# Kernel tuning notes

Hardware: AMD Instinct MI355X
Metric: run time of the kernel (lower is better)

## Reference

```python
import jax, jax.numpy as jnp
import numpy as np

EPS = 1e-12  # tf.nn.l2_normalize epsilon used inside keras CosineSimilarity


def _cos(a, b):
    # keras CosineSimilarity returns -cos; callers negate explicitly.
    an = a / jnp.sqrt(jnp.maximum(jnp.sum(a * a, axis=-1, keepdims=True), EPS))
    bn = b / jnp.sqrt(jnp.maximum(jnp.sum(b * b, axis=-1, keepdims=True), EPS))
    return jnp.sum(an * bn, axis=-1)


def setup_inputs() -> dict:
    key = jax.random.key(0)
    B, S, D, H, N = 1024, 200, 128, 128, 64
    ks = jax.random.split(key, 8)
    X_series = jax.random.normal(ks[0], (B, S, D), jnp.float32)
    pos_series = jax.random.normal(ks[1], (S, D), jnp.float32)
    X_item = jax.random.normal(ks[2], (B, D), jnp.float32)
    origin = jax.random.normal(ks[3], (B, N, D), jnp.float32)  # X_negative
    # contiguous-prefix validity mask (module assumes valid positions form a prefix)
    lengths = jax.random.randint(ks[4], (B,), 1, S + 1)
    valid_mask = jnp.arange(S)[None, :] < lengths[:, None]
    # learned params (GlorotUniform-scale init)
    Wp = jax.random.normal(ks[5], (D, H), jnp.float32) * 0.08
    We = jax.random.normal(ks[6], (D, H), jnp.float32) * 0.08
    z = jax.random.normal(ks[7], (H,), jnp.float32) * 0.1
    return {"X_series": X_series, "pos_series": pos_series, "X_item": X_item,
            "valid_mask": valid_mask, "origin": origin, "Wp": Wp, "We": We, "z": z}


def reference(X_series, pos_series, X_item, valid_mask, origin, Wp, We, z):
    B, S, D = X_series.shape
    # additive tanh attention: z . tanh(X_series @ We + pos_series @ Wp)
    hidden = jnp.tanh(jnp.einsum('bsd,dh->bsh', X_series, We) + (pos_series @ Wp)[None])
    scores = jnp.einsum('bsh,h->bs', hidden, z)
    scores = jnp.where(valid_mask, scores, -jnp.inf)
    attn = jax.nn.softmax(scores, axis=-1)                      # [B,S]
    attentioned = attn[:, :, None] * X_series                    # [B,S,D]
    attention_output = jnp.sum(attentioned, axis=1)              # [B,D]
    inner = jnp.sum(attention_output * X_item, axis=-1, keepdims=True)
    concated = jnp.concatenate([attention_output, inner], axis=1)  # [B,D+1]

    # ---- auxiliary loss ----
    last_idx = jnp.sum(valid_mask.astype(jnp.int32), axis=1) - 1
    last_vec = attentioned[jnp.arange(B), last_idx]              # gather_nd
    new_mask = (jnp.arange(S)[None, :] < last_idx[:, None]).astype(X_series.dtype)
    out_vec = jnp.sum(attentioned * new_mask[:, :, None], axis=1)  # [B,D]
    # keras CosineSimilarity = -cos_sim; then mapped to (x+1)/2 and used as logits
    pos_logits = (-_cos(last_vec, out_vec) + 1.0) / 2.0          # [B]
    neg_logits = (-_cos(origin, out_vec[:, None, :]) + 1.0) / 2.0  # [B,N]
    pos_loss = jax.nn.softplus(-pos_logits)  # sigmoid_xent labels=1
    neg_loss = jax.nn.softplus(neg_logits)   # sigmoid_xent labels=0
    # NB: TF reduces pos_loss over its only axis -> scalar, broadcast-added to [B]
    auxiliary_loss = jnp.sum(pos_loss) + jnp.sum(neg_loss, axis=-1)  # [B]
    return concated, auxiliary_loss
```

## Files before the change

kernel.cpp:

```cpp
#include <hip/hip_runtime.h>
#include <hip/hip_bf16.h>
#include <math.h>

#define B_ 1024
#define S_ 200
#define D_ 128
#define H_ 128
#define N_ 64
#define SP_ 208

typedef __attribute__((ext_vector_type(8))) short short8;
typedef __attribute__((ext_vector_type(8))) __bf16 bf16x8;
typedef __attribute__((ext_vector_type(4))) float floatx4;

static __device__ __forceinline__ float bf2f(unsigned short u) {
    union { unsigned int i; float f; } v; v.i = ((unsigned int)u) << 16; return v.f;
}
static __device__ __forceinline__ unsigned short f2bf(float f) {
    union { float f; unsigned int u; } v; v.f = f;
    unsigned int u = v.u;
    return (unsigned short)((u + 0x7FFFu + ((u >> 16) & 1u)) >> 16);
}
static __device__ __forceinline__ float ld1(const void* p, int isbf, size_t i) {
    return isbf ? bf2f(((const unsigned short*)p)[i]) : ((const float*)p)[i];
}
static __device__ __forceinline__ float fast_tanh(float x) {
    float t = __expf(2.0f * x);
    return 1.0f - 2.0f * __builtin_amdgcn_rcpf(t + 1.0f);
}

__global__ __launch_bounds__(64) void detect_kernel(
    const void* a0, const void* a1, const void* a2, const void* a3,
    const void* a4, const void* a5, const void* a6, const void* a7,
    int* flags)
{
    int bid = blockIdx.x, t = threadIdx.x;
    if (bid == 3) {
        const unsigned char* mb = (const unsigned char*)a3;
        int f = 0;
        for (int i = t; i < 4096; i += 64)
            if ((i & 3) && mb[i]) f = 1;
        for (int off = 32; off; off >>= 1) f |= __shfl_xor(f, off, 64);
        if (t == 0) flags[3] = f;
        return;
    }
    const void* ptrs[8] = {a0, a1, a2, a3, a4, a5, a6, a7};
    const int counts[8] = {B_*S_*D_, S_*D_, B_*D_, 0, B_*N_*D_, D_*H_, D_*H_, H_};
    const unsigned int* w = (const unsigned int*)ptrs[bid];
    int words = counts[bid] / 2; if (words > 1024) words = 1024;
    int pass = 0, tot = 0;
    for (int i = t; i < words; i += 64) {
        unsigned int e = (w[i] >> 7) & 0xFF;
        tot++;
        if (e == 0 || (e >= 96 && e <= 140)) pass++;
    }
    for (int off = 32; off; off >>= 1) {
        pass += __shfl_xor(pass, off, 64);
        tot  += __shfl_xor(tot,  off, 64);
    }
    if (t == 0) flags[bid] = (pass * 4 >= tot * 3) ? 1 : 0;
}

__global__ __launch_bounds__(128) void prep_kernel(
    const void* __restrict__ We, const void* __restrict__ pos,
    const void* __restrict__ Wp, const int* __restrict__ flags,
    unsigned short* __restrict__ WeTf, float* __restrict__ pbT)
{
    int blk = blockIdx.x, t = threadIdx.x;
    __shared__ unsigned short T[128][136];
    __shared__ float prow[D_];
    if (blk == 0) {
        int fWe = flags[6];
        for (int c = t; c < 2048; c += 128) {
            int d = c >> 4, h8 = (c & 15) * 8;
            short8 v;
            if (fWe) {
                v = *(const short8*)((const unsigned short*)We + d * H_ + h8);
            } else {
                const float* p = (const float*)We + d * H_ + h8;
                float4 a = ((const float4*)p)[0], b = ((const float4*)p)[1];
                v[0] = (short)f2bf(a.x); v[1] = (short)f2bf(a.y);
                v[2] = (short)f2bf(a.z); v[3] = (short)f2bf(a.w);
                v[4] = (short)f2bf(b.x); v[5] = (short)f2bf(b.y);
                v[6] = (short)f2bf(b.z); v[7] = (short)f2bf(b.w);
            }
            *(short8*)(&T[d][h8]) = v;
        }
        __syncthreads();
        for (int i = t; i < 2048; i += 128) {
            int frag = i >> 6, ln = i & 63;
            int nt = frag >> 2, kks = frag & 3;
            int h = nt * 16 + (ln & 15);
            int dbase = kks * 32 + (ln >> 4) * 8;
            short8 v;
#pragma unroll
            for (int j = 0; j < 8; ++j) v[j] = (short)T[dbase + j][h];
            *(short8*)(WeTf + (size_t)i * 8) = v;
        }
        for (int i = t; i < H_ * (SP_ - S_); i += 128) {
            int h = i >> 3, s2 = S_ + (i & 7);
            pbT[(size_t)h * SP_ + s2] = 0.f;
        }
    } else {
        int s = blk - 1, h = t;
        prow[h] = ld1(pos, flags[1], (size_t)s * D_ + h);
        __syncthreads();
        float acc = 0.f;
        if (flags[5]) {
            const unsigned short* W = (const unsigned short*)Wp;
            for (int d = 0; d < D_; ++d) acc = fmaf(prow[d], bf2f(W[d * H_ + h]), acc);
        } else {
            const float* W = (const float*)Wp;
            for (int d = 0; d < D_; ++d) acc = fmaf(prow[d], W[d * H_ + h], acc);
        }
        pbT[(size_t)h * SP_ + s] = acc;
    }
}

__global__ __launch_bounds__(512, 4) void fused_kernel(
    const void* __restrict__ Xs, const void* __restrict__ Xitem,
    const void* __restrict__ maskv, const void* __restrict__ origin,
    const unsigned short* __restrict__ WeTf, const float* __restrict__ pbT,
    const void* __restrict__ zv, const int* __restrict__ flags,
    float* __restrict__ pos_loss, float* __restrict__ neg_sum,
    float* __restrict__ out)
{
    int b = blockIdx.x, t = threadIdx.x;
    int wv = t >> 6, lane = t & 63;
    int quad = lane >> 4, mrow = lane & 15;
    int fXs = flags[0], fXi = flags[2], fMk = flags[3], fOr = flags[4], fz = flags[7];

    __shared__ __align__(16) unsigned short Xsh[SP_ * D_];
    __shared__ float smemU[2048];
    __shared__ float attn[256];
    __shared__ float att_out[D_], lastv[D_], outv[D_];
    __shared__ float red[24];
    __shared__ int redi[8];
    __shared__ float sc1s, sc2s, vvs;

    int nn = t >> 3, part = t & 7;
    float o_f[16];
    if (fOr) {
        const unsigned short* p = (const unsigned short*)origin + ((size_t)b * N_ + nn) * D_ + part * 16;
#pragma unroll
        for (int j = 0; j < 2; ++j) {
            uint4 u = *(const uint4*)(p + j * 8);
            o_f[j*8+0] = bf2f((unsigned short)(u.x & 0xffff));
            o_f[j*8+1] = bf2f((unsigned short)(u.x >> 16));
            o_f[j*8+2] = bf2f((unsigned short)(u.y & 0xffff));
            o_f[j*8+3] = bf2f((unsigned short)(u.y >> 16));
            o_f[j*8+4] = bf2f((unsigned short)(u.z & 0xffff));
            o_f[j*8+5] = bf2f((unsigned short)(u.z >> 16));
            o_f[j*8+6] = bf2f((unsigned short)(u.w & 0xffff));
            o_f[j*8+7] = bf2f((unsigned short)(u.w >> 16));
        }
    } else {
        const float* p = (const float*)origin + ((size_t)b * N_ + nn) * D_ + part * 16;
#pragma unroll
        for (int j = 0; j < 4; ++j) {
            float4 v = *(const float4*)(p + j * 4);
            o_f[j*4+0] = v.x; o_f[j*4+1] = v.y; o_f[j*4+2] = v.z; o_f[j*4+3] = v.w;
        }
    }

    for (int i = t; i < SP_ * 16; i += 512) {
        int s = i >> 4, c8 = (i & 15) * 8;
        short8 v;
        if (s >= S_) {
#pragma unroll
            for (int j = 0; j < 8; ++j) v[j] = 0;
        } else if (fXs) {
            v = *(const short8*)((const unsigned short*)Xs + ((size_t)b * S_ + s) * D_ + c8);
        } else {
            const float* p = (const float*)Xs + ((size_t)b * S_ + s) * D_ + c8;
            float4 a = ((const float4*)p)[0], c = ((const float4*)p)[1];
            v[0] = (short)f2bf(a.x); v[1] = (short)f2bf(a.y);
            v[2] = (short)f2bf(a.z); v[3] = (short)f2bf(a.w);
            v[4] = (short)f2bf(c.x); v[5] = (short)f2bf(c.y);
            v[6] = (short)f2bf(c.z); v[7] = (short)f2bf(c.w);
        }
        *(short8*)(Xsh + s * D_ + (c8 ^ ((s & 7) << 3))) = v;
    }

    int nt = wv;
    bf16x8 bfr[4];
#pragma unroll
    for (int kks = 0; kks < 4; ++kks)
        bfr[kks] = __builtin_bit_cast(bf16x8,
            *(const short8*)(WeTf + (size_t)((((nt << 2) + kks) << 6) + lane) * 8));
    float zl = ld1(zv, fz, nt * 16 + mrow);
    const float* pbcol = pbT + (size_t)(nt * 16 + mrow) * SP_;

    __syncthreads();

    float* sp = smemU;
    for (int mt = 0; mt < 13; ++mt) {
        floatx4 acc = {0.f, 0.f, 0.f, 0.f};
        int r = mt * 16 + mrow;
        int rbase = r * D_, rx = (r & 7) << 3;
#pragma unroll
        for (int kks = 0; kks < 4; ++kks) {
            bf16x8 af = __builtin_bit_cast(bf16x8,
                *(const short8*)(Xsh + rbase + ((kks * 32 + quad * 8) ^ rx)));
            acc = __builtin_amdgcn_mfma_f32_16x16x32_bf16(af, bfr[kks], acc, 0, 0, 0);
        }
        float4 pbq = *(const float4*)(pbcol + mt * 16 + quad * 4);
#pragma unroll
        for (int reg = 0; reg < 4; ++reg) {
            float val = fast_tanh(acc[reg] + (&pbq.x)[reg]) * zl;
            val += __shfl_xor(val, 1, 64);
            val += __shfl_xor(val, 2, 64);
            val += __shfl_xor(val, 4, 64);
            val += __shfl_xor(val, 8, 64);
            int s = mt * 16 + quad * 4 + reg;
            if (mrow == 0 && s < S_) sp[nt * SP_ + s] = val;
        }
    }
    __syncthreads();

    float myscore = -INFINITY;
    if (t < S_) {
        float ss = 0.f;
#pragma unroll
        for (int w8 = 0; w8 < 8; ++w8) ss += sp[w8 * SP_ + t];
        myscore = ss;
    }

    int nz = 0;
    if (t < S_)
        nz = fMk ? (((const unsigned char*)maskv)[(size_t)b * S_ + t] != 0)
                 : (((const int*)maskv)[(size_t)b * S_ + t] != 0);
    unsigned long long bal = __ballot(nz);
    if (lane == 0) redi[wv] = __popcll(bal);
    __syncthreads();
    int length = redi[0] + redi[1] + redi[2] + redi[3]
               + redi[4] + redi[5] + redi[6] + redi[7];
    int last = length - 1;

    float sc = (t < length) ? myscore : -INFINITY;
    float m = sc;
    for (int off = 32; off; off >>= 1) m = fmaxf(m, __shfl_xor(m, off, 64));
    if (lane == 0) red[wv] = m;
    __syncthreads();
    if (t == 0) {
        float mm = red[0];
#pragma unroll
        for (int i = 1; i < 8; ++i) mm = fmaxf(mm, red[i]);
        sc1s = mm;
    }
    __syncthreads();
    float e = (t < length) ? expf(sc - sc1s) : 0.f;
    float rr = e;
    for (int off = 32; off; off >>= 1) rr += __shfl_xor(rr, off, 64);
    __syncthreads();
    if (lane == 0) red[wv] = rr;
    __syncthreads();
    if (t == 0) {
        float ssum = 0.f;
#pragma unroll
        for (int i = 0; i < 8; ++i) ssum += red[i];
        sc2s = ssum;
    }
    __syncthreads();
    if (t < 256) attn[t] = e / sc2s;
    __syncthreads();

    float* partial = smemU;
    {
        int spi = t >> 5, d4 = (t & 31) * 4;
        float a0 = 0.f, a1 = 0.f, a2 = 0.f, a3 = 0.f;
        if (fXs) {
            for (int s = spi; s < S_; s += 16) {
                float ww = attn[s];
                uint2 u = *(const uint2*)(Xsh + s * D_ + (d4 ^ ((s & 7) << 3)));
                a0 = fmaf(ww, bf2f((unsigned short)(u.x & 0xffff)), a0);
                a1 = fmaf(ww, bf2f((unsigned short)(u.x >> 16)), a1);
                a2 = fmaf(ww, bf2f((unsigned short)(u.y & 0xffff)), a2);
                a3 = fmaf(ww, bf2f((unsigned short)(u.y >> 16)), a3);
            }
        } else {
            for (int s = spi; s < S_; s += 16) {
                float ww = attn[s];
                float4 u = *(const float4*)((const float*)Xs + ((size_t)b * S_ + s) * D_ + d4);
                a0 = fmaf(ww, u.x, a0); a1 = fmaf(ww, u.y, a1);
                a2 = fmaf(ww, u.z, a2); a3 = fmaf(ww, u.w, a3);
            }
        }
        partial[spi * D_ + d4 + 0] = a0;
        partial[spi * D_ + d4 + 1] = a1;
        partial[spi * D_ + d4 + 2] = a2;
        partial[spi * D_ + d4 + 3] = a3;
    }
    __syncthreads();
    if (t < D_) {
        float v = 0.f;
#pragma unroll
        for (int p = 0; p < 16; ++p) v += partial[p * D_ + t];
        att_out[t] = v;
        float xl = fXs ? bf2f(Xsh[last * D_ + (t ^ ((last & 7) << 3))])
                       : ((const float*)Xs)[((size_t)b * S_ + last) * D_ + t];
        float lv = attn[last] * xl;
        lastv[t] = lv;
        outv[t] = v - lv;
    }
    __syncthreads();

    {
        float pi = (t < D_) ? att_out[t] * ld1(Xitem, fXi, (size_t)b * D_ + t) : 0.f;
        for (int off = 32; off; off >>= 1) pi += __shfl_xor(pi, off, 64);
        if (lane == 0) red[wv] = pi;
        __syncthreads();
        if (t < D_) out[(size_t)b * (D_ + 1) + t] = att_out[t];
        if (t == 0) {
            float s8 = 0.f;
#pragma unroll
            for (int i = 0; i < 8; ++i) s8 += red[i];
            out[(size_t)b * (D_ + 1) + D_] = s8;
        }
        __syncthreads();
    }

    {
        float l_ = (t < D_) ? lastv[t] : 0.f;
        float o_ = (t < D_) ? outv[t] : 0.f;
        float r0 = l_ * l_, r1 = l_ * o_, r2 = o_ * o_;
        for (int off = 32; off; off >>= 1) {
            r0 += __shfl_xor(r0, off, 64);
            r1 += __shfl_xor(r1, off, 64);
            r2 += __shfl_xor(r2, off, 64);
        }
        if (lane == 0) { red[wv] = r0; red[8 + wv] = r1; red[16 + wv] = r2; }
        __syncthreads();
        if (t == 0) {
            float ll = 0.f, lo = 0.f, oo = 0.f;
#pragma unroll
            for (int i = 0; i < 8; ++i) { ll += red[i]; lo += red[8 + i]; oo += red[16 + i]; }
            float cosv = lo / (sqrtf(fmaxf(ll, 1e-12f)) * sqrtf(fmaxf(oo, 1e-12f)));
            float pl = 0.5f * (1.f - cosv);
            pos_loss[b] = log1pf(expf(-pl));
            vvs = oo;
        }
        __syncthreads();
    }

    {
        float* p_oo = smemU;
        float* p_ov = smemU + 512;
        float o_oo = 0.f, o_ov = 0.f;
#pragma unroll
        for (int j = 0; j < 16; ++j) {
            float wv_ = outv[part * 16 + j];
            o_oo = fmaf(o_f[j], o_f[j], o_oo);
            o_ov = fmaf(o_f[j], wv_, o_ov);
        }
        p_oo[part * 64 + nn] = o_oo;
        p_ov[part * 64 + nn] = o_ov;
        __syncthreads();
        if (t < 64) {
            float oo = 0.f, ov = 0.f;
#pragma unroll
            for (int p8 = 0; p8 < 8; ++p8) { oo += p_oo[p8 * 64 + t]; ov += p_ov[p8 * 64 + t]; }
            float cosn = ov / (sqrtf(fmaxf(oo, 1e-12f)) * sqrtf(fmaxf(vvs, 1e-12f)));
            float nl = 0.5f * (1.f - cosn);
            float nloss = log1pf(expf(nl));
            for (int off = 32; off; off >>= 1) nloss += __shfl_xor(nloss, off, 64);
            if (t == 0) neg_sum[b] = nloss;
        }
    }
}

__global__ __launch_bounds__(1024) void final_kernel(
    const float* __restrict__ pos_loss,
    const float* __restrict__ neg_sum,
    float* __restrict__ out)
{
    __shared__ float red[16];
    int t = threadIdx.x;
    float v = pos_loss[t];
    for (int off = 32; off; off >>= 1) v += __shfl_xor(v, off, 64);
    if ((t & 63) == 0) red[t >> 6] = v;
    __syncthreads();
    if (t == 0) {
        float s = 0.f;
#pragma unroll
        for (int i = 0; i < 16; ++i) s += red[i];
        red[0] = s;
    }
    __syncthreads();
    out[(size_t)B_ * (D_ + 1) + t] = red[0] + neg_sum[t];
}

extern "C" void kernel_launch(void* const* d_in, const int* in_sizes, int n_in,
                              void* d_out, int out_size, void* d_ws, size_t ws_size,
                              hipStream_t stream) {
    const void* Xs     = d_in[0];
    const void* pos    = d_in[1];
    const void* Xitem  = d_in[2];
    const void* mask   = d_in[3];
    const void* origin = d_in[4];
    const void* Wp     = d_in[5];
    const void* We     = d_in[6];
    const void* zv     = d_in[7];

    int*   flags    = (int*)d_ws;
    unsigned short* WeTf = (unsigned short*)((char*)d_ws + 128);
    float* pbT      = (float*)((char*)d_ws + 128 + 32768);
    float* pos_loss = pbT + (size_t)H_ * SP_;
    float* neg_sum  = pos_loss + B_;
    float* out = (float*)d_out;

    detect_kernel<<<8, 64, 0, stream>>>(Xs, pos, Xitem, mask, origin, Wp, We, zv, flags);
    prep_kernel<<<201, 128, 0, stream>>>(We, pos, Wp, flags, WeTf, pbT);
    fused_kernel<<<B_, 512, 0, stream>>>(Xs, Xitem, mask, origin, WeTf, pbT, zv, flags,
                                         pos_loss, neg_sum, out);
    final_kernel<<<1, 1024, 0, stream>>>(pos_loss, neg_sum, out);
}
```

Before: 267.1 us.

## Inline dtype detection, pool from LDS, prefetch bias tiles, trim syncs

Drops the separate detect kernel and instead infers input dtypes inside prep and fused kernels from sampled words. The fp32 attention-pooling pass now reads the bf16 copy of X in LDS instead of re-reading fp32 X from global memory. The bf16 X path loads straight into LDS with global_load_lds. The positional bias is stored in an MFMA-fragment layout and prefetched one tile ahead. Softmax and loss reductions are merged to cut barriers. The cost is reduced precision in the pooled output and aux loss for fp32 inputs, because it now uses bf16 X, plus redundant per-block detection reads.

```diff
diff --git a/kernel.cpp b/kernel.cpp
--- a/kernel.cpp
+++ b/kernel.cpp
@@ -13,6 +13,9 @@
 typedef __attribute__((ext_vector_type(8))) __bf16 bf16x8;
 typedef __attribute__((ext_vector_type(4))) float floatx4;
 
+typedef __attribute__((address_space(1))) void gvoid_t;
+typedef __attribute__((address_space(3))) void lvoid_t;
+
 static __device__ __forceinline__ float bf2f(unsigned short u) {
     union { unsigned int i; float f; } v; v.i = ((unsigned int)u) << 16; return v.f;
 }
@@ -28,49 +31,53 @@
     float t = __expf(2.0f * x);
     return 1.0f - 2.0f * __builtin_amdgcn_rcpf(t + 1.0f);
 }
-
-__global__ __launch_bounds__(64) void detect_kernel(
-    const void* a0, const void* a1, const void* a2, const void* a3,
-    const void* a4, const void* a5, const void* a6, const void* a7,
-    int* flags)
-{
-    int bid = blockIdx.x, t = threadIdx.x;
-    if (bid == 3) {
-        const unsigned char* mb = (const unsigned char*)a3;
-        int f = 0;
-        for (int i = t; i < 4096; i += 64)
-            if ((i & 3) && mb[i]) f = 1;
-        for (int off = 32; off; off >>= 1) f |= __shfl_xor(f, off, 64);
-        if (t == 0) flags[3] = f;
-        return;
-    }
-    const void* ptrs[8] = {a0, a1, a2, a3, a4, a5, a6, a7};
-    const int counts[8] = {B_*S_*D_, S_*D_, B_*D_, 0, B_*N_*D_, D_*H_, D_*H_, H_};
-    const unsigned int* w = (const unsigned int*)ptrs[bid];
-    int words = counts[bid] / 2; if (words > 1024) words = 1024;
-    int pass = 0, tot = 0;
-    for (int i = t; i < words; i += 64) {
-        unsigned int e = (w[i] >> 7) & 0xFF;
-        tot++;
-        if (e == 0 || (e >= 96 && e <= 140)) pass++;
-    }
-    for (int off = 32; off; off >>= 1) {
-        pass += __shfl_xor(pass, off, 64);
-        tot  += __shfl_xor(tot,  off, 64);
-    }
-    if (t == 0) flags[bid] = (pass * 4 >= tot * 3) ? 1 : 0;
+static __device__ __forceinline__ void gload_lds16(const void* g, void* l) {
+    __builtin_amdgcn_global_load_lds((const gvoid_t*)g, (lvoid_t*)l, 16, 0, 0);
+}
+
+static __device__ __forceinline__ int detect_wave_256(const void* p) {
+    int lane = threadIdx.x & 63;
+    uint4 w = ((const uint4*)p)[lane];
+    unsigned int ws[4] = {w.x, w.y, w.z, w.w};
+    int pass = 0;
+#pragma unroll
+    for (int k = 0; k < 4; ++k) {
+        unsigned int e = (ws[k] >> 7) & 0xFF;
+        pass += (e == 0 || (e >= 96 && e <= 140)) ? 1 : 0;
+    }
+#pragma unroll
+    for (int off = 32; off; off >>= 1) pass += __shfl_xor(pass, off, 64);
+    return pass * 4 >= 256 * 3;
+}
+static __device__ __forceinline__ int detect_wave_64(const void* p) {
+    int lane = threadIdx.x & 63;
+    unsigned int w = ((const unsigned int*)p)[lane];
+    unsigned int e = (w >> 7) & 0xFF;
+    int pass = (e == 0 || (e >= 96 && e <= 140)) ? 1 : 0;
+#pragma unroll
+    for (int off = 32; off; off >>= 1) pass += __shfl_xor(pass, off, 64);
+    return pass * 4 >= 64 * 3;
+}
+static __device__ __forceinline__ int detect_mask_u8(const void* p) {
+    int lane = threadIdx.x & 63;
+    uint4 w = ((const uint4*)p)[lane];
+    unsigned int x = (w.x | w.y | w.z | w.w) & 0xFFFFFF00u;
+    return (__ballot(x != 0) != 0ULL) ? 1 : 0;
 }
 
 __global__ __launch_bounds__(128) void prep_kernel(
     const void* __restrict__ We, const void* __restrict__ pos,
-    const void* __restrict__ Wp, const int* __restrict__ flags,
-    unsigned short* __restrict__ WeTf, float* __restrict__ pbT)
+    const void* __restrict__ Wp,
+    unsigned short* __restrict__ WeTf, float* __restrict__ pbL)
 {
     int blk = blockIdx.x, t = threadIdx.x;
     __shared__ unsigned short T[128][136];
     __shared__ float prow[D_];
+    __shared__ int fl[2];
     if (blk == 0) {
-        int fWe = flags[6];
+        if (t < 64) { int f = detect_wave_256(We); if (t == 0) fl[0] = f; }
+        __syncthreads();
+        int fWe = fl[0];
         for (int c = t; c < 2048; c += 128) {
             int d = c >> 4, h8 = (c & 15) * 8;
             short8 v;
@@ -97,46 +104,75 @@
             for (int j = 0; j < 8; ++j) v[j] = (short)T[dbase + j][h];
             *(short8*)(WeTf + (size_t)i * 8) = v;
         }
-        for (int i = t; i < H_ * (SP_ - S_); i += 128) {
-            int h = i >> 3, s2 = S_ + (i & 7);
-            pbT[(size_t)h * SP_ + s2] = 0.f;
-        }
     } else {
+        if (t < 64)       { int f = detect_wave_256(pos); if (t == 0)  fl[0] = f; }
+        else if (t < 128) { int f = detect_wave_256(Wp);  if (t == 64) fl[1] = f; }
+        __syncthreads();
+        int fPos = fl[0], fWp = fl[1];
         int s = blk - 1, h = t;
-        prow[h] = ld1(pos, flags[1], (size_t)s * D_ + h);
+        prow[h] = ld1(pos, fPos, (size_t)s * D_ + h);
         __syncthreads();
         float acc = 0.f;
-        if (flags[5]) {
+        if (fWp) {
             const unsigned short* W = (const unsigned short*)Wp;
             for (int d = 0; d < D_; ++d) acc = fmaf(prow[d], bf2f(W[d * H_ + h]), acc);
         } else {
             const float* W = (const float*)Wp;
             for (int d = 0; d < D_; ++d) acc = fmaf(prow[d], W[d * H_ + h], acc);
         }
-        pbT[(size_t)h * SP_ + s] = acc;
+        int mt = s >> 4, qr = s & 15;
+        int idx = (((mt * 8 + (h >> 4)) * 64 + (qr >> 2) * 16 + (h & 15)) << 2) + (qr & 3);
+        pbL[idx] = acc;
     }
 }
 
 __global__ __launch_bounds__(512, 4) void fused_kernel(
     const void* __restrict__ Xs, const void* __restrict__ Xitem,
     const void* __restrict__ maskv, const void* __restrict__ origin,
-    const unsigned short* __restrict__ WeTf, const float* __restrict__ pbT,
-    const void* __restrict__ zv, const int* __restrict__ flags,
+    const unsigned short* __restrict__ WeTf, const float* __restrict__ pbL,
+    const void* __restrict__ zv,
     float* __restrict__ pos_loss, float* __restrict__ neg_sum,
     float* __restrict__ out)
 {
     int b = blockIdx.x, t = threadIdx.x;
     int wv = t >> 6, lane = t & 63;
     int quad = lane >> 4, mrow = lane & 15;
-    int fXs = flags[0], fXi = flags[2], fMk = flags[3], fOr = flags[4], fz = flags[7];
 
     __shared__ __align__(16) unsigned short Xsh[SP_ * D_];
-    __shared__ float smemU[2048];
+    __shared__ __align__(16) float partial[4096];
+    __shared__ float red4[512];
     __shared__ float attn[256];
-    __shared__ float att_out[D_], lastv[D_], outv[D_];
-    __shared__ float red[24];
+    __shared__ float outv[D_];
+    __shared__ float red[32];
     __shared__ int redi[8];
-    __shared__ float sc1s, sc2s, vvs;
+
+    int fXs = detect_wave_256(Xs);
+    int fXi = detect_wave_256(Xitem);
+    int fOr = detect_wave_256(origin);
+    int fz  = detect_wave_64(zv);
+    int fMk = detect_mask_u8(maskv);
+
+    if (fXs) {
+        const unsigned short* gb = (const unsigned short*)Xs + (size_t)b * (S_ * D_);
+        for (int i = t; i < S_ * 16; i += 512) {
+            int s = i >> 4, c8 = (i & 15) * 8;
+            int cs = c8 ^ ((s & 7) << 3);
+            gload_lds16(gb + (size_t)s * D_ + cs, Xsh + (size_t)i * 8);
+        }
+    } else {
+        const float* gb = (const float*)Xs + (size_t)b * (S_ * D_);
+        for (int i = t; i < S_ * 16; i += 512) {
+            int s = i >> 4, c8 = (i & 15) * 8;
+            const float* p = gb + (size_t)s * D_ + c8;
+            float4 a = ((const float4*)p)[0], c = ((const float4*)p)[1];
+            short8 v;
+            v[0] = (short)f2bf(a.x); v[1] = (short)f2bf(a.y);
+            v[2] = (short)f2bf(a.z); v[3] = (short)f2bf(a.w);
+            v[4] = (short)f2bf(c.x); v[5] = (short)f2bf(c.y);
+            v[6] = (short)f2bf(c.z); v[7] = (short)f2bf(c.w);
+            *(short8*)(Xsh + s * D_ + (c8 ^ ((s & 7) << 3))) = v;
+        }
+    }
 
     int nn = t >> 3, part = t & 7;
     float o_f[16];
@@ -162,25 +198,11 @@
             o_f[j*4+0] = v.x; o_f[j*4+1] = v.y; o_f[j*4+2] = v.z; o_f[j*4+3] = v.w;
         }
     }
-
-    for (int i = t; i < SP_ * 16; i += 512) {
-        int s = i >> 4, c8 = (i & 15) * 8;
-        short8 v;
-        if (s >= S_) {
-#pragma unroll
-            for (int j = 0; j < 8; ++j) v[j] = 0;
-        } else if (fXs) {
-            v = *(const short8*)((const unsigned short*)Xs + ((size_t)b * S_ + s) * D_ + c8);
-        } else {
-            const float* p = (const float*)Xs + ((size_t)b * S_ + s) * D_ + c8;
-            float4 a = ((const float4*)p)[0], c = ((const float4*)p)[1];
-            v[0] = (short)f2bf(a.x); v[1] = (short)f2bf(a.y);
-            v[2] = (short)f2bf(a.z); v[3] = (short)f2bf(a.w);
-            v[4] = (short)f2bf(c.x); v[5] = (short)f2bf(c.y);
-            v[6] = (short)f2bf(c.z); v[7] = (short)f2bf(c.w);
-        }
-        *(short8*)(Xsh + s * D_ + (c8 ^ ((s & 7) << 3))) = v;
-    }
+    float xiv = (t < D_) ? ld1(Xitem, fXi, (size_t)b * D_ + t) : 0.f;
+    int nz = 0;
+    if (t < S_)
+        nz = fMk ? (((const unsigned char*)maskv)[(size_t)b * S_ + t] != 0)
+                 : (((const int*)maskv)[(size_t)b * S_ + t] != 0);
 
     int nt = wv;
     bf16x8 bfr[4];
@@ -189,12 +211,16 @@
         bfr[kks] = __builtin_bit_cast(bf16x8,
             *(const short8*)(WeTf + (size_t)((((nt << 2) + kks) << 6) + lane) * 8));
     float zl = ld1(zv, fz, nt * 16 + mrow);
-    const float* pbcol = pbT + (size_t)(nt * 16 + mrow) * SP_;
-
-    __syncthreads();
-
-    float* sp = smemU;
+    const float4* pbw = (const float4*)pbL + nt * 64 + lane;
+    float4 pbc = pbw[0];
+
+    asm volatile("s_waitcnt vmcnt(0)" ::: "memory");
+    __syncthreads();
+
+    float* sp = partial;
     for (int mt = 0; mt < 13; ++mt) {
+        float4 pbn = pbc;
+        if (mt < 12) pbn = pbw[(size_t)(mt + 1) * 512];
         floatx4 acc = {0.f, 0.f, 0.f, 0.f};
         int r = mt * 16 + mrow;
         int rbase = r * D_, rx = (r & 7) << 3;
@@ -204,10 +230,9 @@
                 *(const short8*)(Xsh + rbase + ((kks * 32 + quad * 8) ^ rx)));
             acc = __builtin_amdgcn_mfma_f32_16x16x32_bf16(af, bfr[kks], acc, 0, 0, 0);
         }
-        float4 pbq = *(const float4*)(pbcol + mt * 16 + quad * 4);
 #pragma unroll
         for (int reg = 0; reg < 4; ++reg) {
-            float val = fast_tanh(acc[reg] + (&pbq.x)[reg]) * zl;
+            float val = fast_tanh(acc[reg] + (&pbc.x)[reg]) * zl;
             val += __shfl_xor(val, 1, 64);
             val += __shfl_xor(val, 2, 64);
             val += __shfl_xor(val, 4, 64);
@@ -215,6 +240,7 @@
             int s = mt * 16 + quad * 4 + reg;
             if (mrow == 0 && s < S_) sp[nt * SP_ + s] = val;
         }
+        pbc = pbn;
     }
     __syncthreads();
 
@@ -225,127 +251,92 @@
         for (int w8 = 0; w8 < 8; ++w8) ss += sp[w8 * SP_ + t];
         myscore = ss;
     }
-
-    int nz = 0;
-    if (t < S_)
-        nz = fMk ? (((const unsigned char*)maskv)[(size_t)b * S_ + t] != 0)
-                 : (((const int*)maskv)[(size_t)b * S_ + t] != 0);
     unsigned long long bal = __ballot(nz);
-    if (lane == 0) redi[wv] = __popcll(bal);
+    float scv = nz ? myscore : -INFINITY;
+    float m = scv;
+#pragma unroll
+    for (int off = 32; off; off >>= 1) m = fmaxf(m, __shfl_xor(m, off, 64));
+    if (lane == 0) { red[wv] = m; redi[wv] = __popcll(bal); }
     __syncthreads();
     int length = redi[0] + redi[1] + redi[2] + redi[3]
                + redi[4] + redi[5] + redi[6] + redi[7];
     int last = length - 1;
-
-    float sc = (t < length) ? myscore : -INFINITY;
-    float m = sc;
-    for (int off = 32; off; off >>= 1) m = fmaxf(m, __shfl_xor(m, off, 64));
-    if (lane == 0) red[wv] = m;
-    __syncthreads();
-    if (t == 0) {
-        float mm = red[0];
-#pragma unroll
-        for (int i = 1; i < 8; ++i) mm = fmaxf(mm, red[i]);
-        sc1s = mm;
-    }
-    __syncthreads();
-    float e = (t < length) ? expf(sc - sc1s) : 0.f;
+    float mglob = red[0];
+#pragma unroll
+    for (int i = 1; i < 8; ++i) mglob = fmaxf(mglob, red[i]);
+    float e = nz ? expf(myscore - mglob) : 0.f;
     float rr = e;
+#pragma unroll
     for (int off = 32; off; off >>= 1) rr += __shfl_xor(rr, off, 64);
-    __syncthreads();
-    if (lane == 0) red[wv] = rr;
-    __syncthreads();
-    if (t == 0) {
-        float ssum = 0.f;
-#pragma unroll
-        for (int i = 0; i < 8; ++i) ssum += red[i];
-        sc2s = ssum;
-    }
-    __syncthreads();
-    if (t < 256) attn[t] = e / sc2s;
-    __syncthreads();
-
-    float* partial = smemU;
+    if (lane == 0) red[8 + wv] = rr;
+    __syncthreads();
+    float ssum = red[8] + red[9] + red[10] + red[11]
+               + red[12] + red[13] + red[14] + red[15];
+    if (t < 256) attn[t] = e / ssum;
+    __syncthreads();
+
     {
-        int spi = t >> 5, d4 = (t & 31) * 4;
+        int spi = t >> 4;
+        int d8 = (t & 15) * 8;
         float a0 = 0.f, a1 = 0.f, a2 = 0.f, a3 = 0.f;
-        if (fXs) {
-            for (int s = spi; s < S_; s += 16) {
-                float ww = attn[s];
-                uint2 u = *(const uint2*)(Xsh + s * D_ + (d4 ^ ((s & 7) << 3)));
-                a0 = fmaf(ww, bf2f((unsigned short)(u.x & 0xffff)), a0);
-                a1 = fmaf(ww, bf2f((unsigned short)(u.x >> 16)), a1);
-                a2 = fmaf(ww, bf2f((unsigned short)(u.y & 0xffff)), a2);
-                a3 = fmaf(ww, bf2f((unsigned short)(u.y >> 16)), a3);
-            }
-        } else {
-            for (int s = spi; s < S_; s += 16) {
-                float ww = attn[s];
-                float4 u = *(const float4*)((const float*)Xs + ((size_t)b * S_ + s) * D_ + d4);
-                a0 = fmaf(ww, u.x, a0); a1 = fmaf(ww, u.y, a1);
-                a2 = fmaf(ww, u.z, a2); a3 = fmaf(ww, u.w, a3);
-            }
-        }
-        partial[spi * D_ + d4 + 0] = a0;
-        partial[spi * D_ + d4 + 1] = a1;
-        partial[spi * D_ + d4 + 2] = a2;
-        partial[spi * D_ + d4 + 3] = a3;
-    }
-    __syncthreads();
+        float a4 = 0.f, a5 = 0.f, a6 = 0.f, a7 = 0.f;
+        for (int s = spi; s < S_; s += 32) {
+            float ww = attn[s];
+            short8 v2 = *(const short8*)(Xsh + s * D_ + (d8 ^ ((s & 7) << 3)));
+            a0 = fmaf(ww, bf2f((unsigned short)v2[0]), a0);
+            a1 = fmaf(ww, bf2f((unsigned short)v2[1]), a1);
+            a2 = fmaf(ww, bf2f((unsigned short)v2[2]), a2);
+            a3 = fmaf(ww, bf2f((unsigned short)v2[3]), a3);
+            a4 = fmaf(ww, bf2f((unsigned short)v2[4]), a4);
+            a5 = fmaf(ww, bf2f((unsigned short)v2[5]), a5);
+            a6 = fmaf(ww, bf2f((unsigned short)v2[6]), a6);
+            a7 = fmaf(ww, bf2f((unsigned short)v2[7]), a7);
+        }
+        float4 w0 = {a0, a1, a2, a3}, w1 = {a4, a5, a6, a7};
+        *(float4*)(partial + spi * D_ + d8)     = w0;
+        *(float4*)(partial + spi * D_ + d8 + 4) = w1;
+    }
+    __syncthreads();
+    {
+        int g = t >> 7, d = t & 127;
+        float sgp = 0.f;
+#pragma unroll
+        for (int p = 0; p < 8; ++p) sgp += partial[(g * 8 + p) * D_ + d];
+        red4[g * D_ + d] = sgp;
+    }
+    __syncthreads();
+
     if (t < D_) {
-        float v = 0.f;
-#pragma unroll
-        for (int p = 0; p < 16; ++p) v += partial[p * D_ + t];
-        att_out[t] = v;
-        float xl = fXs ? bf2f(Xsh[last * D_ + (t ^ ((last & 7) << 3))])
-                       : ((const float*)Xs)[((size_t)b * S_ + last) * D_ + t];
+        float att = red4[t] + red4[D_ + t] + red4[2 * D_ + t] + red4[3 * D_ + t];
+        float xl = bf2f(Xsh[last * D_ + (t ^ ((last & 7) << 3))]);
         float lv = attn[last] * xl;
-        lastv[t] = lv;
-        outv[t] = v - lv;
-    }
-    __syncthreads();
-
-    {
-        float pi = (t < D_) ? att_out[t] * ld1(Xitem, fXi, (size_t)b * D_ + t) : 0.f;
-        for (int off = 32; off; off >>= 1) pi += __shfl_xor(pi, off, 64);
-        if (lane == 0) red[wv] = pi;
-        __syncthreads();
-        if (t < D_) out[(size_t)b * (D_ + 1) + t] = att_out[t];
-        if (t == 0) {
-            float s8 = 0.f;
-#pragma unroll
-            for (int i = 0; i < 8; ++i) s8 += red[i];
-            out[(size_t)b * (D_ + 1) + D_] = s8;
-        }
-        __syncthreads();
-    }
-
-    {
-        float l_ = (t < D_) ? lastv[t] : 0.f;
-        float o_ = (t < D_) ? outv[t] : 0.f;
-        float r0 = l_ * l_, r1 = l_ * o_, r2 = o_ * o_;
+        float ov = att - lv;
+        outv[t] = ov;
+        out[(size_t)b * (D_ + 1) + t] = att;
+        float r0 = att * xiv;
+        float r1 = lv * lv, r2 = lv * ov, r3 = ov * ov;
+#pragma unroll
         for (int off = 32; off; off >>= 1) {
             r0 += __shfl_xor(r0, off, 64);
             r1 += __shfl_xor(r1, off, 64);
             r2 += __shfl_xor(r2, off, 64);
-        }
-        if (lane == 0) { red[wv] = r0; red[8 + wv] = r1; red[16 + wv] = r2; }
-        __syncthreads();
-        if (t == 0) {
-            float ll = 0.f, lo = 0.f, oo = 0.f;
-#pragma unroll
-            for (int i = 0; i < 8; ++i) { ll += red[i]; lo += red[8 + i]; oo += red[16 + i]; }
-            float cosv = lo / (sqrtf(fmaxf(ll, 1e-12f)) * sqrtf(fmaxf(oo, 1e-12f)));
-            float pl = 0.5f * (1.f - cosv);
-            pos_loss[b] = log1pf(expf(-pl));
-            vvs = oo;
-        }
-        __syncthreads();
+            r3 += __shfl_xor(r3, off, 64);
+        }
+        if (lane == 0) { red[wv] = r0; red[8 + wv] = r1; red[16 + wv] = r2; red[24 + wv] = r3; }
+    }
+    __syncthreads();
+    float vv = red[24] + red[25];
+    if (t == 0) {
+        out[(size_t)b * (D_ + 1) + D_] = red[0] + red[1];
+        float ll = red[8] + red[9], lo = red[16] + red[17];
+        float cosv = lo / (sqrtf(fmaxf(ll, 1e-12f)) * sqrtf(fmaxf(vv, 1e-12f)));
+        float pl = 0.5f * (1.f - cosv);
+        pos_loss[b] = log1pf(expf(-pl));
     }
 
     {
-        float* p_oo = smemU;
-        float* p_ov = smemU + 512;
+        float* p_oo = partial;
+        float* p_ov = partial + 512;
         float o_oo = 0.f, o_ov = 0.f;
 #pragma unroll
         for (int j = 0; j < 16; ++j) {
@@ -357,12 +348,13 @@
         p_ov[part * 64 + nn] = o_ov;
         __syncthreads();
         if (t < 64) {
-            float oo = 0.f, ov = 0.f;
-#pragma unroll
-            for (int p8 = 0; p8 < 8; ++p8) { oo += p_oo[p8 * 64 + t]; ov += p_ov[p8 * 64 + t]; }
-            float cosn = ov / (sqrtf(fmaxf(oo, 1e-12f)) * sqrtf(fmaxf(vvs, 1e-12f)));
+            float oo = 0.f, ov2 = 0.f;
+#pragma unroll
+            for (int p8 = 0; p8 < 8; ++p8) { oo += p_oo[p8 * 64 + t]; ov2 += p_ov[p8 * 64 + t]; }
+            float cosn = ov2 / (sqrtf(fmaxf(oo, 1e-12f)) * sqrtf(fmaxf(vv, 1e-12f)));
             float nl = 0.5f * (1.f - cosn);
             float nloss = log1pf(expf(nl));
+#pragma unroll
             for (int off = 32; off; off >>= 1) nloss += __shfl_xor(nloss, off, 64);
             if (t == 0) neg_sum[b] = nloss;
         }
@@ -402,16 +394,14 @@
     const void* We     = d_in[6];
     const void* zv     = d_in[7];
 
-    int*   flags    = (int*)d_ws;
-    unsigned short* WeTf = (unsigned short*)((char*)d_ws + 128);
-    float* pbT      = (float*)((char*)d_ws + 128 + 32768);
-    float* pos_loss = pbT + (size_t)H_ * SP_;
+    unsigned short* WeTf = (unsigned short*)d_ws;
+    float* pbL      = (float*)((char*)d_ws + 32768);
+    float* pos_loss = pbL + 13 * 8 * 64 * 4;
     float* neg_sum  = pos_loss + B_;
     float* out = (float*)d_out;
 
-    detect_kernel<<<8, 64, 0, stream>>>(Xs, pos, Xitem, mask, origin, Wp, We, zv, flags);
-    prep_kernel<<<201, 128, 0, stream>>>(We, pos, Wp, flags, WeTf, pbT);
-    fused_kernel<<<B_, 512, 0, stream>>>(Xs, Xitem, mask, origin, WeTf, pbT, zv, flags,
+    prep_kernel<<<201, 128, 0, stream>>>(We, pos, Wp, WeTf, pbL);
+    fused_kernel<<<B_, 512, 0, stream>>>(Xs, Xitem, mask, origin, WeTf, pbL, zv,
                                          pos_loss, neg_sum, out);
     final_kernel<<<1, 1024, 0, stream>>>(pos_loss, neg_sum, out);
 }
```

Measured after the change: 236.5 us. 11.5% less time.
